# Optimization experiments

Hardware: AMD Instinct MI355X
Metric: run time of the kernel (lower is better)

## Reference

```python
import jax, jax.numpy as jnp
import numpy as np

BLOCK_LEN = 64  # chunk length l


def setup_inputs() -> dict:
    key = jax.random.key(0)
    k1, k2, k3 = jax.random.split(key, 3)
    b, s, h, p, n = 8, 4096, 16, 64, 64
    X = jax.random.normal(k1, (b, s, h, p), jnp.float32)
    # A must be negative for numerically stable decays (exp(cumsum diffs) <= 1),
    # matching real Mamba2 where A_log parameterizes a negative decay rate.
    A = -0.1 * jnp.abs(jax.random.normal(k2, (b, s, h), jnp.float32))
    B = jax.random.normal(k3, (b, s, h, n), jnp.float32)
    return {"X": X, "A": A, "B": B}


def reference(X, A, B):
    L = BLOCK_LEN
    b, s, h, p = X.shape
    n = B.shape[-1]
    c = s // L  # number of chunks

    # b (c l) ... -> b c l ...
    Xb = X.reshape(b, c, L, h, p)
    Bb = B.reshape(b, c, L, h, n)
    Ab = jnp.transpose(A.reshape(b, c, L, h), (0, 3, 1, 2))  # (b, h, c, l)

    A_cumsum = jnp.cumsum(Ab, axis=-1)  # (b, h, c, l)

    # Fused decay-einsum: states[b,c,h,p,n] =
    #   sum_l B[b,c,l,h,n] * exp(A_cumsum[b,h,c,-1] - A_cumsum[b,h,c,l]) * X[b,c,l,h,p]
    decay_states = jnp.exp(A_cumsum[..., -1:] - A_cumsum)  # (b, h, c, l)
    states = jnp.einsum('bclhn,bhcl,bclhp->bchpn', Bb, decay_states, Xb)

    # Prepend zero initial states along chunk dim -> (b, c+1, h, p, n)
    states = jnp.concatenate([jnp.zeros_like(states[:, :1]), states], axis=1)

    # Inter-chunk recurrence via exp(segsum(padded chunk totals)).
    padded_A = jnp.pad(A_cumsum[..., -1], ((0, 0), (0, 0), (1, 0)))  # (b, h, c+1)
    cs = jnp.cumsum(padded_A, axis=-1)
    Z = c + 1
    diff = cs[..., :, None] - cs[..., None, :]  # (b, h, Z, Z), row - col
    mask = jnp.tril(jnp.ones((Z, Z), dtype=bool))  # row >= col
    decay_chunk = jnp.where(mask, jnp.exp(diff), 0.0)  # (b, h, Z, Z)

    new_states = jnp.einsum('bhzc,bchpn->bzhpn', decay_chunk, states)
    return new_states[:, -1]  # (b, h, p, n)
```

## Files before the change

kernel.cpp:

```cpp
#include <hip/hip_runtime.h>
#include <math.h>


constexpr int Bn = 8;
constexpr int S  = 4096;
constexpr int H  = 16;
constexpr int Pp = 64;
constexpr int Nn = 64;
constexpr int SEG  = 128;
constexpr int NSEG = S / SEG;

__global__ __launch_bounds__(256) void seg_sums(const float* __restrict__ A,
                                                float* __restrict__ ss) {
  const int bb  = blockIdx.x >> 5;
  const int seg = blockIdx.x & 31;
  __shared__ float lds[SEG * H];
  const float* src = A + ((size_t)bb * S + (size_t)seg * SEG) * H;
  const int tid = threadIdx.x;
  #pragma unroll
  for (int i = 0; i < 2; ++i)
    ((float4*)lds)[tid + i * 256] = ((const float4*)src)[tid + i * 256];
  __syncthreads();
  if (tid < H) {
    float s = 0.f;
    for (int t = 0; t < SEG; ++t) s += lds[t * H + tid];
    ss[((size_t)bb * NSEG + seg) * H + tid] = s;
  }
}

__global__ __launch_bounds__(256) void seg_scan(const float* __restrict__ ss,
                                                float* __restrict__ pfx,
                                                float* __restrict__ tot) {
  const int pid = threadIdx.x;
  if (pid >= Bn * H) return;
  const int bb = pid >> 4, h = pid & 15;
  float run = 0.f;
  for (int s = 0; s < NSEG; ++s) {
    pfx[(size_t)pid * NSEG + s] = run;
    run += ss[((size_t)bb * NSEG + s) * H + h];
  }
  tot[pid] = run;
}

__global__ __launch_bounds__(256) void outer_k(const float* __restrict__ X,
                                               const float* __restrict__ Bm,
                                               const float* __restrict__ A,
                                               const float* __restrict__ pfx,
                                               const float* __restrict__ tot,
                                               float* __restrict__ part, int SC) {
  const int blk  = blockIdx.x;
  const int pair = blk / SC, sc = blk % SC;
  const int bb = pair >> 4, hh = pair & 15;
  const int tid = threadIdx.x, w = tid >> 6, lane = tid & 63;
  const int TPW = S / (SC * 4);
  const int t0  = sc * (S / SC) + w * TPW;
  const int r = lane >> 3, c = lane & 7;

  float acc[8][8];
  #pragma unroll
  for (int i = 0; i < 8; ++i)
    #pragma unroll
    for (int j = 0; j < 8; ++j) acc[i][j] = 0.f;

  float run = pfx[(size_t)pair * NSEG + t0 / SEG];
  const float total = tot[pair];

  const float* Arow = A + ((size_t)bb * S + t0) * H + hh;
  const float* Xrow = X + (((size_t)bb * S + t0) * H + hh) * Pp + r * 8;
  const float* Brow = Bm + (((size_t)bb * S + t0) * H + hh) * Nn + c * 8;
  constexpr size_t TS = (size_t)H * Pp;

  #pragma unroll 2
  for (int t = 0; t < TPW; ++t) {
    const float a = Arow[(size_t)t * H];
    run += a;
    const float wgt = __expf(total - run);
    const float4 x0 = *(const float4*)(Xrow + (size_t)t * TS);
    const float4 x1 = *(const float4*)(Xrow + (size_t)t * TS + 4);
    const float4 b0 = *(const float4*)(Brow + (size_t)t * TS);
    const float4 b1 = *(const float4*)(Brow + (size_t)t * TS + 4);
    const float xs[8] = {x0.x * wgt, x0.y * wgt, x0.z * wgt, x0.w * wgt,
                         x1.x * wgt, x1.y * wgt, x1.z * wgt, x1.w * wgt};
    const float bs[8] = {b0.x, b0.y, b0.z, b0.w, b1.x, b1.y, b1.z, b1.w};
    #pragma unroll
    for (int i = 0; i < 8; ++i)
      #pragma unroll
      for (int j = 0; j < 8; ++j)
        acc[i][j] = fmaf(xs[i], bs[j], acc[i][j]);
  }

  __shared__ float red[2][4096];
  if (w >= 2) {
    #pragma unroll
    for (int i = 0; i < 8; ++i)
      #pragma unroll
      for (int j = 0; j < 8; ++j) red[w - 2][(i * 8 + j) * 64 + lane] = acc[i][j];
  }
  __syncthreads();
  if (w < 2) {
    #pragma unroll
    for (int i = 0; i < 8; ++i)
      #pragma unroll
      for (int j = 0; j < 8; ++j) acc[i][j] += red[w][(i * 8 + j) * 64 + lane];
  }
  __syncthreads();
  if (w == 1) {
    #pragma unroll
    for (int i = 0; i < 8; ++i)
      #pragma unroll
      for (int j = 0; j < 8; ++j) red[0][(i * 8 + j) * 64 + lane] = acc[i][j];
  }
  __syncthreads();
  if (w == 0) {
    float* base = part + (size_t)blk * 4096;
    #pragma unroll
    for (int i = 0; i < 8; ++i) {
      #pragma unroll
      for (int j = 0; j < 8; ++j) acc[i][j] += red[0][(i * 8 + j) * 64 + lane];
      *(float4*)(base + (r * 8 + i) * 64 + c * 8)     =
          make_float4(acc[i][0], acc[i][1], acc[i][2], acc[i][3]);
      *(float4*)(base + (r * 8 + i) * 64 + c * 8 + 4) =
          make_float4(acc[i][4], acc[i][5], acc[i][6], acc[i][7]);
    }
  }
}

__global__ __launch_bounds__(256) void reduce_k(const float* __restrict__ part,
                                                float* __restrict__ out, int SC) {
  const int idx  = blockIdx.x * 256 + threadIdx.x;
  const int pair = idx >> 10;
  const int off  = (idx & 1023) * 4;
  float4 s = make_float4(0.f, 0.f, 0.f, 0.f);
  for (int sc = 0; sc < SC; ++sc) {
    const float4 v = *(const float4*)(part + ((size_t)(pair * SC + sc)) * 4096 + off);
    s.x += v.x; s.y += v.y; s.z += v.z; s.w += v.w;
  }
  *(float4*)(out + (size_t)pair * 4096 + off) = s;
}

extern "C" void kernel_launch(void* const* d_in, const int* in_sizes, int n_in,
                              void* d_out, int out_size, void* d_ws, size_t ws_size,
                              hipStream_t stream) {
  const float* X = (const float*)d_in[0];
  const float* A = (const float*)d_in[1];
  const float* B = (const float*)d_in[2];
  float* out = (float*)d_out;

  int SC = 8;
  const size_t misc = (size_t)(Bn * NSEG * H + Bn * H * NSEG + Bn * H) * sizeof(float);
  while (SC > 1 && (size_t)Bn * H * SC * 4096 * sizeof(float) + misc > ws_size) SC >>= 1;

  float* part = (float*)d_ws;
  float* ss   = part + (size_t)Bn * H * SC * 4096;
  float* pfx  = ss + (size_t)Bn * NSEG * H;
  float* tot  = pfx + (size_t)Bn * H * NSEG;

  seg_sums<<<Bn * NSEG, 256, 0, stream>>>(A, ss);
  seg_scan<<<1, 256, 0, stream>>>(ss, pfx, tot);
  outer_k<<<Bn * H * SC, 256, 0, stream>>>(X, B, A, pfx, tot, part, SC);
  reduce_k<<<(Bn * H * Pp * Nn) / 4 / 256, 256, 0, stream>>>(part, out, SC);
}
```

Baseline: 341.9 us.

## Stage X/B tiles via async LDS loads, fuse reduce with atomics, precompute prefix sums

Replaces direct global loads in the outer-product kernel with double-buffered global_load_lds staging of X and B tiles, and computes per-timestep cumulative sums of A in a separate scan kernel. The segment prefix scan moves into the main kernel as a wave shuffle scan. The partial-sum reduction kernel is removed in favour of atomicAdd into a zeroed output. This aims to raise memory throughput and cut launches, at the cost of atomic contention, nondeterministic summation order and an extra memset.

```diff
diff --git a/kernel.cpp b/kernel.cpp
--- a/kernel.cpp
+++ b/kernel.cpp
@@ -5,56 +5,86 @@
 constexpr int Bn = 8;
 constexpr int S  = 4096;
 constexpr int H  = 16;
-constexpr int Pp = 64;
-constexpr int Nn = 64;
 constexpr int SEG  = 128;
 constexpr int NSEG = S / SEG;
+constexpr int SC  = 8;
+constexpr int TPB = S / SC;
+constexpr int TB  = 32;
+constexpr int NST = TPB / TB;
 
-__global__ __launch_bounds__(256) void seg_sums(const float* __restrict__ A,
-                                                float* __restrict__ ss) {
-  const int bb  = blockIdx.x >> 5;
-  const int seg = blockIdx.x & 31;
-  __shared__ float lds[SEG * H];
-  const float* src = A + ((size_t)bb * S + (size_t)seg * SEG) * H;
-  const int tid = threadIdx.x;
-  #pragma unroll
-  for (int i = 0; i < 2; ++i)
-    ((float4*)lds)[tid + i * 256] = ((const float4*)src)[tid + i * 256];
-  __syncthreads();
-  if (tid < H) {
-    float s = 0.f;
-    for (int t = 0; t < SEG; ++t) s += lds[t * H + tid];
-    ss[((size_t)bb * NSEG + seg) * H + tid] = s;
-  }
+#define AS1 __attribute__((address_space(1)))
+#define AS3 __attribute__((address_space(3)))
+
+static __device__ __forceinline__ void g2lds16(const float* g, float* l) {
+  __builtin_amdgcn_global_load_lds((const AS1 unsigned int*)g, (AS3 unsigned int*)l, 16, 0, 0);
+}
+static __device__ __forceinline__ void g2lds4(const float* g, float* l) {
+  __builtin_amdgcn_global_load_lds((const AS1 unsigned int*)g, (AS3 unsigned int*)l, 4, 0, 0);
 }
 
-__global__ __launch_bounds__(256) void seg_scan(const float* __restrict__ ss,
-                                                float* __restrict__ pfx,
-                                                float* __restrict__ tot) {
-  const int pid = threadIdx.x;
-  if (pid >= Bn * H) return;
-  const int bb = pid >> 4, h = pid & 15;
-  float run = 0.f;
-  for (int s = 0; s < NSEG; ++s) {
-    pfx[(size_t)pid * NSEG + s] = run;
-    run += ss[((size_t)bb * NSEG + s) * H + h];
+__global__ __launch_bounds__(256) void scanA(const float* __restrict__ A,
+                                             float* __restrict__ Plb,
+                                             float* __restrict__ ss) {
+  __shared__ float Al[SEG * 17];
+  __shared__ float sp[16][17];
+  const int bb = blockIdx.x >> 5, seg = blockIdx.x & 31;
+  const int tid = threadIdx.x;
+  const float* src = A + ((size_t)bb * S + (size_t)seg * SEG) * H;
+  #pragma unroll
+  for (int k = 0; k < 2; ++k) {
+    const int f = tid + k * 256;
+    const float4 v = ((const float4*)src)[f];
+    const int t = f >> 2, h0 = (f & 3) * 4;
+    Al[t * 17 + h0 + 0] = v.x; Al[t * 17 + h0 + 1] = v.y;
+    Al[t * 17 + h0 + 2] = v.z; Al[t * 17 + h0 + 3] = v.w;
   }
-  tot[pid] = run;
+  __syncthreads();
+  const int h = tid >> 4, j = tid & 15;
+  float vals[8], run = 0.f;
+  #pragma unroll
+  for (int k = 0; k < 8; ++k) { run += Al[(j * 8 + k) * 17 + h]; vals[k] = run; }
+  sp[h][j] = run;
+  __syncthreads();
+  float pre = 0.f, tot = 0.f;
+  #pragma unroll
+  for (int jj = 0; jj < 16; ++jj) { const float x = sp[h][jj]; tot += x; if (jj < j) pre += x; }
+  if (j == 0) ss[((size_t)bb * NSEG + seg) * H + h] = tot;
+  float* Wp = Plb + ((size_t)(bb * H + h)) * S + seg * SEG + j * 8;
+  *(float4*)(Wp)     = make_float4(pre + vals[0], pre + vals[1], pre + vals[2], pre + vals[3]);
+  *(float4*)(Wp + 4) = make_float4(pre + vals[4], pre + vals[5], pre + vals[6], pre + vals[7]);
 }
 
-__global__ __launch_bounds__(256) void outer_k(const float* __restrict__ X,
-                                               const float* __restrict__ Bm,
-                                               const float* __restrict__ A,
-                                               const float* __restrict__ pfx,
-                                               const float* __restrict__ tot,
-                                               float* __restrict__ part, int SC) {
-  const int blk  = blockIdx.x;
-  const int pair = blk / SC, sc = blk % SC;
+__global__ __launch_bounds__(256, 4) void outer_k(const float* __restrict__ X,
+                                                  const float* __restrict__ Bm,
+                                                  const float* __restrict__ Plb,
+                                                  const float* __restrict__ ss,
+                                                  float* __restrict__ out) {
+  __shared__ float smem[4096 + 4096 + 128];
+  float* Xs = smem;
+  float* Bs = smem + 4096;
+  float* Pl = smem + 8192;
+
+  const int blk = blockIdx.x;
+  const int pair = blk >> 3, sc = blk & 7;
   const int bb = pair >> 4, hh = pair & 15;
   const int tid = threadIdx.x, w = tid >> 6, lane = tid & 63;
-  const int TPW = S / (SC * 4);
-  const int t0  = sc * (S / SC) + w * TPW;
+  const int tstart = sc * TPB;
   const int r = lane >> 3, c = lane & 7;
+
+  float segv = (lane < NSEG) ? ss[((size_t)bb * NSEG + lane) * H + hh] : 0.f;
+  float incl = segv;
+  #pragma unroll
+  for (int off = 1; off < NSEG; off <<= 1) {
+    const float u = __shfl_up(incl, off, 64);
+    if (lane >= off) incl += u;
+  }
+  const float tot = __shfl(incl, NSEG - 1, 64);
+  const float pe  = incl - segv;
+
+  constexpr size_t RS = (size_t)H * 64;
+  const float* Xb = X  + (((size_t)bb * S + tstart) * H + hh) * 64;
+  const float* Bb = Bm + (((size_t)bb * S + tstart) * H + hh) * 64;
+  const float* Pb = Plb + (size_t)pair * S + tstart;
 
   float acc[8][8];
   #pragma unroll
@@ -62,80 +92,82 @@
     #pragma unroll
     for (int j = 0; j < 8; ++j) acc[i][j] = 0.f;
 
-  float run = pfx[(size_t)pair * NSEG + t0 / SEG];
-  const float total = tot[pair];
+  #define ISSUE(s_, buf_) do {                                                  \
+    const size_t tg = (size_t)((s_) * TB + w * 8) * RS;                         \
+    float* dx = Xs + (buf_) * 2048 + w * 512;                                   \
+    float* db = Bs + (buf_) * 2048 + w * 512;                                   \
+    _Pragma("unroll")                                                           \
+    for (int k = 0; k < 2; ++k) {                                               \
+      const int f = k * 64 + lane;                                              \
+      const size_t go = tg + (size_t)(f >> 4) * RS + (size_t)(f & 15) * 4;      \
+      g2lds16(Xb + go, dx + k * 256);                                           \
+      g2lds16(Bb + go, db + k * 256);                                           \
+    }                                                                           \
+    if (w == 0) g2lds4(Pb + (s_) * TB + (lane & 31), Pl + (buf_) * 64);         \
+  } while (0)
 
-  const float* Arow = A + ((size_t)bb * S + t0) * H + hh;
-  const float* Xrow = X + (((size_t)bb * S + t0) * H + hh) * Pp + r * 8;
-  const float* Brow = Bm + (((size_t)bb * S + t0) * H + hh) * Nn + c * 8;
-  constexpr size_t TS = (size_t)H * Pp;
+  ISSUE(0, 0);
+  for (int s = 0; s < NST; ++s) {
+    __syncthreads();
+    if (s + 1 < NST) ISSUE(s + 1, (s + 1) & 1);
+    const int seg = (tstart + s * TB) >> 7;
+    const float cm = tot - __shfl(pe, seg, 64);
+    const float* xb = Xs + (s & 1) * 2048;
+    const float* bv = Bs + (s & 1) * 2048;
+    const float* pl = Pl + (s & 1) * 64;
+    #pragma unroll
+    for (int it = 0; it < 8; ++it) {
+      const int tt = it * 4 + w;
+      const float wgt = __expf(cm - pl[tt]);
+      const float4 x0 = *(const float4*)(xb + tt * 64 + r * 8);
+      const float4 x1 = *(const float4*)(xb + tt * 64 + r * 8 + 4);
+      const float4 b0 = *(const float4*)(bv + tt * 64 + c * 8);
+      const float4 b1 = *(const float4*)(bv + tt * 64 + c * 8 + 4);
+      const float xs[8] = {x0.x * wgt, x0.y * wgt, x0.z * wgt, x0.w * wgt,
+                           x1.x * wgt, x1.y * wgt, x1.z * wgt, x1.w * wgt};
+      const float bs[8] = {b0.x, b0.y, b0.z, b0.w, b1.x, b1.y, b1.z, b1.w};
+      #pragma unroll
+      for (int i = 0; i < 8; ++i)
+        #pragma unroll
+        for (int j = 0; j < 8; ++j)
+          acc[i][j] = fmaf(xs[i], bs[j], acc[i][j]);
+    }
+  }
+  __syncthreads();
 
-  #pragma unroll 2
-  for (int t = 0; t < TPW; ++t) {
-    const float a = Arow[(size_t)t * H];
-    run += a;
-    const float wgt = __expf(total - run);
-    const float4 x0 = *(const float4*)(Xrow + (size_t)t * TS);
-    const float4 x1 = *(const float4*)(Xrow + (size_t)t * TS + 4);
-    const float4 b0 = *(const float4*)(Brow + (size_t)t * TS);
-    const float4 b1 = *(const float4*)(Brow + (size_t)t * TS + 4);
-    const float xs[8] = {x0.x * wgt, x0.y * wgt, x0.z * wgt, x0.w * wgt,
-                         x1.x * wgt, x1.y * wgt, x1.z * wgt, x1.w * wgt};
-    const float bs[8] = {b0.x, b0.y, b0.z, b0.w, b1.x, b1.y, b1.z, b1.w};
-    #pragma unroll
-    for (int i = 0; i < 8; ++i)
-      #pragma unroll
-      for (int j = 0; j < 8; ++j)
-        acc[i][j] = fmaf(xs[i], bs[j], acc[i][j]);
-  }
-
-  __shared__ float red[2][4096];
+  float* red = smem;
   if (w >= 2) {
     #pragma unroll
     for (int i = 0; i < 8; ++i)
       #pragma unroll
-      for (int j = 0; j < 8; ++j) red[w - 2][(i * 8 + j) * 64 + lane] = acc[i][j];
+      for (int j = 0; j < 8; ++j) red[(w - 2) * 4096 + (i * 8 + j) * 64 + lane] = acc[i][j];
   }
   __syncthreads();
   if (w < 2) {
     #pragma unroll
     for (int i = 0; i < 8; ++i)
       #pragma unroll
-      for (int j = 0; j < 8; ++j) acc[i][j] += red[w][(i * 8 + j) * 64 + lane];
+      for (int j = 0; j < 8; ++j) acc[i][j] += red[w * 4096 + (i * 8 + j) * 64 + lane];
   }
   __syncthreads();
   if (w == 1) {
     #pragma unroll
     for (int i = 0; i < 8; ++i)
       #pragma unroll
-      for (int j = 0; j < 8; ++j) red[0][(i * 8 + j) * 64 + lane] = acc[i][j];
+      for (int j = 0; j < 8; ++j) red[(i * 8 + j) * 64 + lane] = acc[i][j];
   }
   __syncthreads();
   if (w == 0) {
-    float* base = part + (size_t)blk * 4096;
+    float* op = out + (size_t)pair * 4096;
     #pragma unroll
-    for (int i = 0; i < 8; ++i) {
+    for (int i = 0; i < 8; ++i)
       #pragma unroll
-      for (int j = 0; j < 8; ++j) acc[i][j] += red[0][(i * 8 + j) * 64 + lane];
-      *(float4*)(base + (r * 8 + i) * 64 + c * 8)     =
-          make_float4(acc[i][0], acc[i][1], acc[i][2], acc[i][3]);
-      *(float4*)(base + (r * 8 + i) * 64 + c * 8 + 4) =
-          make_float4(acc[i][4], acc[i][5], acc[i][6], acc[i][7]);
-    }
+      for (int j = 0; j < 8; ++j) {
+        const float v = acc[i][j] + red[(i * 8 + j) * 64 + lane];
+        atomicAdd(&op[(r * 8 + i) * 64 + c * 8 + j], v);
+      }
   }
-}
-
-__global__ __launch_bounds__(256) void reduce_k(const float* __restrict__ part,
-                                                float* __restrict__ out, int SC) {
-  const int idx  = blockIdx.x * 256 + threadIdx.x;
-  const int pair = idx >> 10;
-  const int off  = (idx & 1023) * 4;
-  float4 s = make_float4(0.f, 0.f, 0.f, 0.f);
-  for (int sc = 0; sc < SC; ++sc) {
-    const float4 v = *(const float4*)(part + ((size_t)(pair * SC + sc)) * 4096 + off);
-    s.x += v.x; s.y += v.y; s.z += v.z; s.w += v.w;
-  }
-  *(float4*)(out + (size_t)pair * 4096 + off) = s;
+  #undef ISSUE
 }
 
 extern "C" void kernel_launch(void* const* d_in, const int* in_sizes, int n_in,
@@ -146,17 +178,10 @@
   const float* B = (const float*)d_in[2];
   float* out = (float*)d_out;
 
-  int SC = 8;
-  const size_t misc = (size_t)(Bn * NSEG * H + Bn * H * NSEG + Bn * H) * sizeof(float);
-  while (SC > 1 && (size_t)Bn * H * SC * 4096 * sizeof(float) + misc > ws_size) SC >>= 1;
+  float* Plb = (float*)d_ws;
+  float* ss  = Plb + (size_t)Bn * H * S;
 
-  float* part = (float*)d_ws;
-  float* ss   = part + (size_t)Bn * H * SC * 4096;
-  float* pfx  = ss + (size_t)Bn * NSEG * H;
-  float* tot  = pfx + (size_t)Bn * H * NSEG;
-
-  seg_sums<<<Bn * NSEG, 256, 0, stream>>>(A, ss);
-  seg_scan<<<1, 256, 0, stream>>>(ss, pfx, tot);
-  outer_k<<<Bn * H * SC, 256, 0, stream>>>(X, B, A, pfx, tot, part, SC);
-  reduce_k<<<(Bn * H * Pp * Nn) / 4 / 256, 256, 0, stream>>>(part, out, SC);
+  hipMemsetAsync(d_out, 0, (size_t)out_size * sizeof(float), stream);
+  scanA<<<Bn * NSEG, 256, 0, stream>>>(A, Plb, ss);
+  outer_k<<<Bn * H * SC, 256, 0, stream>>>(X, B, Plb, ss, out);
 }
```

After: 650.6 us. +90.3%, slower.
